# Kernel tuning notes

Measured on AMD Instinct MI355X. Metric: run time of the kernel, lower is better.

## Reference

```python
import jax, jax.numpy as jnp
import numpy as np

N, D_FEAT, D, H, L = 2048, 128, 256, 8, 2
DH = D // H
E = 65536
NUM_EDGE_TYPES = 8
MAX_DIST = 10
MAX_DEGREE = 512
D_FF = 4 * D
D_OUT = 128
EPS = 1e-5


def _layernorm(x, g, b):
    mu = jnp.mean(x, axis=-1, keepdims=True)
    var = jnp.mean(jnp.square(x - mu), axis=-1, keepdims=True)
    return (x - mu) * jax.lax.rsqrt(var + EPS) * g + b


def setup_inputs() -> dict:
    key = jax.random.key(0)
    ks = jax.random.split(key, 32)
    inp = {
        "x": jax.random.normal(ks[0], (N, D_FEAT), dtype=jnp.float32),
        "edge_index": jax.random.randint(ks[1], (2, E), 0, N),
        "edge_types": jax.random.randint(ks[2], (E,), 0, NUM_EDGE_TYPES),
        "pos_encoding": jax.random.uniform(ks[3], (N, N), dtype=jnp.float32),
    }
    def xavier(k, shape):
        fan_in, fan_out = shape[0], shape[1]
        lim = float(np.sqrt(6.0 / (fan_in + fan_out)))
        return jax.random.uniform(k, shape, jnp.float32, -lim, lim)
    inp["W_emb"] = xavier(ks[4], (D_FEAT, D)); inp["b_emb"] = jnp.zeros((D,), jnp.float32)
    # stacked per-layer params, stored as [in, out] so y = x @ W + b
    inp["Wq"] = jnp.stack([xavier(jax.random.fold_in(ks[5], l), (D, D)) for l in range(L)])
    inp["Wk"] = jnp.stack([xavier(jax.random.fold_in(ks[6], l), (D, D)) for l in range(L)])
    inp["Wv"] = jnp.stack([xavier(jax.random.fold_in(ks[7], l), (D, D)) for l in range(L)])
    inp["Wo"] = jnp.stack([xavier(jax.random.fold_in(ks[8], l), (D, D)) for l in range(L)])
    for nm in ("bq", "bk", "bv", "bo"):
        inp[nm] = jnp.zeros((L, D), jnp.float32)
    inp["spd_table"] = 0.02 * jax.random.normal(ks[9], (L, MAX_DIST + 1, H), dtype=jnp.float32)
    inp["edge_table"] = 0.02 * jax.random.normal(ks[10], (L, NUM_EDGE_TYPES, H), dtype=jnp.float32)
    inp["din_emb"] = 0.02 * jax.random.normal(ks[11], (L, MAX_DEGREE + 1, D), dtype=jnp.float32)
    inp["dout_emb"] = 0.02 * jax.random.normal(ks[12], (L, MAX_DEGREE + 1, D), dtype=jnp.float32)
    inp["ln1_g"] = jnp.ones((L, D), jnp.float32); inp["ln1_b"] = jnp.zeros((L, D), jnp.float32)
    inp["ln2_g"] = jnp.ones((L, D), jnp.float32); inp["ln2_b"] = jnp.zeros((L, D), jnp.float32)
    inp["W1"] = jnp.stack([xavier(jax.random.fold_in(ks[13], l), (D, D_FF)) for l in range(L)])
    inp["b1"] = jnp.zeros((L, D_FF), jnp.float32)
    inp["W2"] = jnp.stack([xavier(jax.random.fold_in(ks[14], l), (D_FF, D)) for l in range(L)])
    inp["b2"] = jnp.zeros((L, D), jnp.float32)
    inp["W_out"] = xavier(ks[15], (D, D_OUT)); inp["b_out"] = jnp.zeros((D_OUT,), jnp.float32)
    return inp


def _forward(x, edge_index, edge_types, pos_encoding,
             W_emb, b_emb, Wq, bq, Wk, bk, Wv, bv, Wo, bo,
             spd_table, edge_table, din_emb, dout_emb,
             ln1_g, ln1_b, ln2_g, ln2_b, W1, b1, W2, b2, W_out, b_out):
    src, dst = edge_index[0], edge_index[1]
    ones = jnp.ones((E,), jnp.int32)
    deg_out = jnp.clip(jax.ops.segment_sum(ones, src, num_segments=N), 0, MAX_DEGREE)
    deg_in = jnp.clip(jax.ops.segment_sum(ones, dst, num_segments=N), 0, MAX_DEGREE)
    # SPD bucket matrix [N, N] (int), shared across layers
    spd_bucket = jnp.clip(pos_encoding[:, :N] * MAX_DIST + 0.5, 0, MAX_DIST).astype(jnp.int32)

    h = x @ W_emb + b_emb  # node embedding; dropout=0 (eval)
    scale = 1.0 / np.sqrt(DH)
    for l in range(L):
        # centrality encoding
        h = h + din_emb[l][deg_in] + dout_emb[l][deg_out]
        xn = _layernorm(h, ln1_g[l], ln1_b[l])
        q = (xn @ Wq[l] + bq[l]).reshape(N, H, DH).transpose(1, 0, 2)  # [H,N,DH]
        k = (xn @ Wk[l] + bk[l]).reshape(N, H, DH).transpose(1, 0, 2)
        v = (xn @ Wv[l] + bv[l]).reshape(N, H, DH).transpose(1, 0, 2)
        # attention bias [H, N, N]: SPD table gather + per-edge scatter-add
        bias = spd_table[l][spd_bucket].transpose(2, 0, 1)
        e_bias = edge_table[l][edge_types]  # [E, H]
        bias = bias.at[:, src, dst].add(e_bias.T)
        scores = jnp.einsum('hnd,hmd->hnm', q, k) * scale + bias
        attn = jax.nn.softmax(scores, axis=-1)
        attn_out = jnp.einsum('hnm,hmd->hnd', attn, v).transpose(1, 0, 2).reshape(N, D)
        h = h + attn_out @ Wo[l] + bo[l]
        y = _layernorm(h, ln2_g[l], ln2_b[l])
        y = jax.nn.gelu(y @ W1[l] + b1[l], approximate=False) @ W2[l] + b2[l]
        h = h + y
    return h @ W_out + b_out


def reference(x, edge_index, edge_types, pos_encoding,
              W_emb, b_emb, Wq, bq, Wk, bk, Wv, bv, Wo, bo,
              spd_table, edge_table, din_emb, dout_emb,
              ln1_g, ln1_b, ln2_g, ln2_b, W1, b1, W2, b2, W_out, b_out):
    return _forward(x, edge_index, edge_types, pos_encoding,
                    W_emb, b_emb, Wq, bq, Wk, bk, Wv, bv, Wo, bo,
                    spd_table, edge_table, din_emb, dout_emb,
                    ln1_g, ln1_b, ln2_g, ln2_b, W1, b1, W2, b2, W_out, b_out)
```

## Files before the change

kernel.cpp:

```cpp
#include <hip/hip_runtime.h>
#include <math.h>

#define N_NODES 2048
#define D_MODEL 256
#define D_FEAT 128
#define NHEAD 8
#define DH 32
#define NLAYER 2
#define NEDGE 65536
#define D_FF 1024
#define D_OUT 128
#define MAXDEG 512
#define JSPLIT 4

typedef __attribute__((ext_vector_type(8))) short short8;
typedef __attribute__((ext_vector_type(4))) float f32x4;
typedef __attribute__((ext_vector_type(4))) unsigned short u16x4;

__device__ __forceinline__ unsigned short f2bf(float f) {
    unsigned u = __float_as_uint(f);
    unsigned r = (u + 0x7FFFu + ((u >> 16) & 1u)) >> 16;
    return (unsigned short)r;
}

template <int CTRL>
__device__ __forceinline__ float dpp_ror(float x) {
    return __int_as_float(__builtin_amdgcn_update_dpp(0, __float_as_int(x), CTRL, 0xf, 0xf, false));
}

__global__ void degree_hist_kernel(const int* __restrict__ ei,
                                   int* __restrict__ deg_out, int* __restrict__ deg_in,
                                   unsigned* __restrict__ hist) {
    int e = blockIdx.x * 256 + threadIdx.x;
    if (e < NEDGE) {
        int src = ei[e], dst = ei[NEDGE + e];
        atomicAdd(&deg_out[src], 1);
        atomicAdd(&deg_in[dst], 1);
        atomicAdd(&hist[(src >> 6) * 2048 + dst], 1);
    }
}

__global__ void edge_scan1_kernel(const unsigned* __restrict__ hist,
                                  unsigned* __restrict__ offsets, unsigned* __restrict__ blocksum) {
    __shared__ unsigned tmp[256];
    int t = threadIdx.x;
    int g = blockIdx.x * 256 + t;
    unsigned v = hist[g];
    tmp[t] = v; __syncthreads();
    for (int off = 1; off < 256; off <<= 1) {
        unsigned u = (t >= off) ? tmp[t - off] : 0;
        __syncthreads();
        tmp[t] += u;
        __syncthreads();
    }
    offsets[g] = tmp[t] - v;
    if (t == 255) blocksum[blockIdx.x] = tmp[255];
}

__global__ void edge_scan2_kernel(unsigned* __restrict__ blocksum) {
    __shared__ unsigned tmp[256];
    int t = threadIdx.x;
    unsigned v = blocksum[t];
    tmp[t] = v; __syncthreads();
    for (int off = 1; off < 256; off <<= 1) {
        unsigned u = (t >= off) ? tmp[t - off] : 0;
        __syncthreads();
        tmp[t] += u;
        __syncthreads();
    }
    blocksum[t] = tmp[t] - v;
}

__global__ void edge_scan3_kernel(const unsigned* __restrict__ blocksum,
                                  unsigned* __restrict__ offsets, unsigned* __restrict__ cursor) {
    int g = blockIdx.x * 256 + threadIdx.x;
    unsigned o = offsets[g] + blocksum[blockIdx.x];
    offsets[g] = o; cursor[g] = o;
    if (g == 0) offsets[65536] = NEDGE;
}

__global__ void edge_scatter_kernel(const int* __restrict__ ei, const int* __restrict__ etypes,
                                    unsigned* __restrict__ cursor, unsigned* __restrict__ packed) {
    int e = blockIdx.x * 256 + threadIdx.x;
    if (e < NEDGE) {
        int src = ei[e], dst = ei[NEDGE + e];
        int key = (src >> 6) * 2048 + dst;
        unsigned pos = atomicAdd(&cursor[key], 1);
        packed[pos] = (unsigned)dst | ((unsigned)(src & 63) << 11) | ((unsigned)etypes[e] << 17);
    }
}

__global__ void bucket_kernel(const float* __restrict__ pos, unsigned char* __restrict__ bucket) {
    int i = blockIdx.x * 256 + threadIdx.x;
    float4 p = *(const float4*)&pos[(size_t)i * 4];
    unsigned b0 = (unsigned)fminf(fmaxf(p.x * 10.f + 0.5f, 0.f), 10.f);
    unsigned b1 = (unsigned)fminf(fmaxf(p.y * 10.f + 0.5f, 0.f), 10.f);
    unsigned b2 = (unsigned)fminf(fmaxf(p.z * 10.f + 0.5f, 0.f), 10.f);
    unsigned b3 = (unsigned)fminf(fmaxf(p.w * 10.f + 0.5f, 0.f), 10.f);
    ((unsigned*)bucket)[i] = b0 | (b1 << 8) | (b2 << 16) | (b3 << 24);
}

__global__ void centrality_ln_kernel(float* __restrict__ h,
                                     const float* __restrict__ din_l,
                                     const float* __restrict__ dout_l,
                                     const int* __restrict__ deg_in,
                                     const int* __restrict__ deg_out,
                                     const float* __restrict__ g,
                                     const float* __restrict__ b,
                                     unsigned short* __restrict__ y) {
    int row = blockIdx.x;
    int tid = threadIdx.x;
    int di = min(deg_in[row], MAXDEG);
    int dn = min(deg_out[row], MAXDEG);
    float v = h[row * D_MODEL + tid] + din_l[di * D_MODEL + tid] + dout_l[dn * D_MODEL + tid];
    h[row * D_MODEL + tid] = v;
    __shared__ float red[256];
    red[tid] = v; __syncthreads();
    for (int s = 128; s > 0; s >>= 1) { if (tid < s) red[tid] += red[tid + s]; __syncthreads(); }
    float mu = red[0] * (1.0f / D_MODEL);
    __syncthreads();
    float d = v - mu;
    red[tid] = d * d; __syncthreads();
    for (int s = 128; s > 0; s >>= 1) { if (tid < s) red[tid] += red[tid + s]; __syncthreads(); }
    float rstd = rsqrtf(red[0] * (1.0f / D_MODEL) + 1e-5f);
    y[row * D_MODEL + tid] = f2bf(d * rstd * g[tid] + b[tid]);
}

__global__ void layernorm_kernel(const float* __restrict__ x,
                                 const float* __restrict__ g,
                                 const float* __restrict__ b,
                                 unsigned short* __restrict__ y) {
    int row = blockIdx.x;
    int tid = threadIdx.x;
    float v = x[row * D_MODEL + tid];
    __shared__ float red[256];
    red[tid] = v; __syncthreads();
    for (int s = 128; s > 0; s >>= 1) { if (tid < s) red[tid] += red[tid + s]; __syncthreads(); }
    float mu = red[0] * (1.0f / D_MODEL);
    __syncthreads();
    float d = v - mu;
    red[tid] = d * d; __syncthreads();
    for (int s = 128; s > 0; s >>= 1) { if (tid < s) red[tid] += red[tid + s]; __syncthreads(); }
    float rstd = rsqrtf(red[0] * (1.0f / D_MODEL) + 1e-5f);
    y[row * D_MODEL + tid] = f2bf(d * rstd * g[tid] + b[tid]);
}

__device__ __forceinline__ void wt_tile(const float* __restrict__ W, unsigned short* __restrict__ Wt,
                                        int K, int Nc, int n0, int k0, int tid,
                                        unsigned short (*tile)[33]) {
    int r = tid >> 3, cg = (tid & 7) * 4;
    float4 w4 = *(const float4*)&W[(size_t)(k0 + r) * Nc + n0 + cg];
    tile[r][cg + 0] = f2bf(w4.x); tile[r][cg + 1] = f2bf(w4.y);
    tile[r][cg + 2] = f2bf(w4.z); tile[r][cg + 3] = f2bf(w4.w);
    __syncthreads();
    int c = tid >> 3, rg = (tid & 7) * 4;
    u16x4 o;
    #pragma unroll
    for (int j = 0; j < 4; j++) o[j] = tile[rg + j][c];
    *(u16x4*)&Wt[(size_t)(n0 + c) * K + k0 + rg] = o;
}

__global__ void wt_all_kernel(const float* __restrict__ Wq, const float* __restrict__ Wk,
                              const float* __restrict__ Wv, const float* __restrict__ Wo,
                              const float* __restrict__ W1, const float* __restrict__ W2,
                              const float* __restrict__ W_emb, const float* __restrict__ W_out,
                              const float* __restrict__ bq, const float* __restrict__ bk,
                              const float* __restrict__ bv,
                              unsigned short* __restrict__ qkvt, unsigned short* __restrict__ wot,
                              unsigned short* __restrict__ w1t, unsigned short* __restrict__ w2t,
                              unsigned short* __restrict__ wembt, unsigned short* __restrict__ woutt,
                              float* __restrict__ bqkv) {
    __shared__ unsigned short tile[32][33];
    int b = blockIdx.x, tid = threadIdx.x;
    if (b < 512) {
        int z = b >> 6, t = b & 63;
        int l = z >> 2, which = z & 3;
        const float* W = (which == 0 ? Wq : which == 1 ? Wk : which == 2 ? Wv : Wo) + (size_t)l * 65536;
        unsigned short* dst = (which < 3) ? qkvt + (size_t)l * 196608 + which * 65536
                                          : wot + (size_t)l * 65536;
        wt_tile(W, dst, 256, 256, (t & 7) * 32, (t >> 3) * 32, tid, tile);
    } else if (b < 1024) {
        int b2 = b - 512, l = b2 >> 8, t = b2 & 255;
        wt_tile(W1 + (size_t)l * D_MODEL * D_FF, w1t + (size_t)l * D_MODEL * D_FF,
                D_MODEL, D_FF, (t & 31) * 32, (t >> 5) * 32, tid, tile);
    } else if (b < 1536) {
        int b3 = b - 1024, l = b3 >> 8, t = b3 & 255;
        wt_tile(W2 + (size_t)l * D_FF * D_MODEL, w2t + (size_t)l * D_FF * D_MODEL,
                D_FF, D_MODEL, (t & 7) * 32, (t >> 3) * 32, tid, tile);
    } else if (b < 1568) {
        int b4 = b - 1536;
        wt_tile(W_emb, wembt, D_FEAT, D_MODEL, (b4 & 7) * 32, (b4 >> 3) * 32, tid, tile);
    } else if (b < 1600) {
        int b5 = b - 1568;
        wt_tile(W_out, woutt, D_MODEL, D_OUT, (b5 & 3) * 32, (b5 >> 2) * 32, tid, tile);
    } else {
        int i = (b - 1600) * 256 + tid;
        if (i < NLAYER * 768) {
            int l = i / 768, j = i % 768;
            const float* src = j < 256 ? bq : j < 512 ? bk : bv;
            bqkv[i] = src[l * 256 + (j & 255)];
        }
    }
}

template <int ACT, bool RESID, bool OUTBF16, bool AFP32>
__global__ void gemm_mfma_kernel(const void* __restrict__ Av,
                                 const unsigned short* __restrict__ Wt,
                                 const float* __restrict__ bias,
                                 float* __restrict__ C, unsigned short* __restrict__ Cb,
                                 int Nc, int K) {
    __shared__ __align__(16) unsigned short As[32][72];
    __shared__ __align__(16) unsigned short Bs[64][72];
    const unsigned short* A16 = (const unsigned short*)Av;
    const float* A32 = (const float*)Av;
    int tid = threadIdx.x;
    int m0 = blockIdx.y * 32, n0 = blockIdx.x * 64;
    int w = tid >> 6, lane = tid & 63;
    int rg = (w & 1) * 16, cg = (w >> 1) * 32;
    int m = lane & 15, quad = lane >> 4;
    f32x4 acc[2] = {{0.f, 0.f, 0.f, 0.f}, {0.f, 0.f, 0.f, 0.f}};
    int ar = tid >> 3, ac = (tid & 7) * 8;
    uint4 ra; float4 fa0, fa1; uint4 rb0, rb1;
    if (AFP32) {
        fa0 = *(const float4*)&A32[(size_t)(m0 + ar) * K + ac];
        fa1 = *(const float4*)&A32[(size_t)(m0 + ar) * K + ac + 4];
    } else {
        ra = *(const uint4*)&A16[(size_t)(m0 + ar) * K + ac];
    }
    rb0 = *(const uint4*)&Wt[(size_t)(n0 + ar) * K + ac];
    rb1 = *(const uint4*)&Wt[(size_t)(n0 + 32 + ar) * K + ac];
    for (int k0 = 0; k0 < K; k0 += 64) {
        if (AFP32) {
            u16x4 t0 = {f2bf(fa0.x), f2bf(fa0.y), f2bf(fa0.z), f2bf(fa0.w)};
            u16x4 t1 = {f2bf(fa1.x), f2bf(fa1.y), f2bf(fa1.z), f2bf(fa1.w)};
            *(u16x4*)&As[ar][ac] = t0;
            *(u16x4*)&As[ar][ac + 4] = t1;
        } else {
            *(uint4*)&As[ar][ac] = ra;
        }
        *(uint4*)&Bs[ar][ac] = rb0;
        *(uint4*)&Bs[ar + 32][ac] = rb1;
        __syncthreads();
        int kn = k0 + 64;
        if (kn < K) {
            if (AFP32) {
                fa0 = *(const float4*)&A32[(size_t)(m0 + ar) * K + kn + ac];
                fa1 = *(const float4*)&A32[(size_t)(m0 + ar) * K + kn + ac + 4];
            } else {
                ra = *(const uint4*)&A16[(size_t)(m0 + ar) * K + kn + ac];
            }
            rb0 = *(const uint4*)&Wt[(size_t)(n0 + ar) * K + kn + ac];
            rb1 = *(const uint4*)&Wt[(size_t)(n0 + 32 + ar) * K + kn + ac];
        }
        #pragma unroll
        for (int ks = 0; ks < 2; ks++) {
            short8 a = *(const short8*)&As[rg + m][ks * 32 + quad * 8];
            #pragma unroll
            for (int t = 0; t < 2; t++) {
                short8 b = *(const short8*)&Bs[cg + t * 16 + m][ks * 32 + quad * 8];
                acc[t] = __builtin_amdgcn_mfma_f32_16x16x32_bf16(a, b, acc[t], 0, 0, 0);
            }
        }
        __syncthreads();
    }
    #pragma unroll
    for (int t = 0; t < 2; t++) {
        #pragma unroll
        for (int reg = 0; reg < 4; reg++) {
            int row = m0 + rg + quad * 4 + reg;
            int col = n0 + cg + t * 16 + m;
            float val = acc[t][reg] + bias[col];
            if (ACT == 1) val = val * 0.5f * (1.0f + erff(val * 0.7071067811865476f));
            size_t idx = (size_t)row * Nc + col;
            if (RESID) val += C[idx];
            if (OUTBF16) Cb[idx] = f2bf(val);
            else C[idx] = val;
        }
    }
}

template <int ACT, bool VBT>
__global__ void gemm64_kernel(const unsigned short* __restrict__ A,
                              const unsigned short* __restrict__ Wt,
                              const float* __restrict__ bias,
                              unsigned short* __restrict__ Cb,
                              unsigned short* __restrict__ vbt,
                              int Nc, int K) {
    __shared__ __align__(16) unsigned short As[64][72];
    __shared__ __align__(16) unsigned short Bs[64][72];
    int tid = threadIdx.x;
    int m0 = blockIdx.y * 64, n0 = blockIdx.x * 64;
    int w = tid >> 6, lane = tid & 63;
    int wr = (w & 1) * 32, wc = (w >> 1) * 32;
    int m = lane & 15, quad = lane >> 4;
    f32x4 acc[2][2] = {{{0.f,0.f,0.f,0.f},{0.f,0.f,0.f,0.f}},{{0.f,0.f,0.f,0.f},{0.f,0.f,0.f,0.f}}};
    int sr = tid >> 2, sg = (tid & 3) * 16;
    uint4 a0 = *(const uint4*)&A[(size_t)(m0 + sr) * K + sg];
    uint4 a1 = *(const uint4*)&A[(size_t)(m0 + sr) * K + sg + 8];
    uint4 b0 = *(const uint4*)&Wt[(size_t)(n0 + sr) * K + sg];
    uint4 b1 = *(const uint4*)&Wt[(size_t)(n0 + sr) * K + sg + 8];
    for (int k0 = 0; k0 < K; k0 += 64) {
        *(uint4*)&As[sr][sg] = a0;
        *(uint4*)&As[sr][sg + 8] = a1;
        *(uint4*)&Bs[sr][sg] = b0;
        *(uint4*)&Bs[sr][sg + 8] = b1;
        __syncthreads();
        int kn = k0 + 64;
        if (kn < K) {
            a0 = *(const uint4*)&A[(size_t)(m0 + sr) * K + kn + sg];
            a1 = *(const uint4*)&A[(size_t)(m0 + sr) * K + kn + sg + 8];
            b0 = *(const uint4*)&Wt[(size_t)(n0 + sr) * K + kn + sg];
            b1 = *(const uint4*)&Wt[(size_t)(n0 + sr) * K + kn + sg + 8];
        }
        #pragma unroll
        for (int kh = 0; kh < 2; kh++) {
            short8 x0 = *(const short8*)&As[wr + m][kh * 32 + quad * 8];
            short8 x1 = *(const short8*)&As[wr + 16 + m][kh * 32 + quad * 8];
            short8 y0 = *(const short8*)&Bs[wc + m][kh * 32 + quad * 8];
            short8 y1 = *(const short8*)&Bs[wc + 16 + m][kh * 32 + quad * 8];
            acc[0][0] = __builtin_amdgcn_mfma_f32_16x16x32_bf16(x0, y0, acc[0][0], 0, 0, 0);
            acc[0][1] = __builtin_amdgcn_mfma_f32_16x16x32_bf16(x0, y1, acc[0][1], 0, 0, 0);
            acc[1][0] = __builtin_amdgcn_mfma_f32_16x16x32_bf16(x1, y0, acc[1][0], 0, 0, 0);
            acc[1][1] = __builtin_amdgcn_mfma_f32_16x16x32_bf16(x1, y1, acc[1][1], 0, 0, 0);
        }
        __syncthreads();
    }
    #pragma unroll
    for (int mt = 0; mt < 2; mt++) {
        #pragma unroll
        for (int nt = 0; nt < 2; nt++) {
            #pragma unroll
            for (int reg = 0; reg < 4; reg++) {
                int row = m0 + wr + mt * 16 + quad * 4 + reg;
                int col = n0 + wc + nt * 16 + m;
                float val = acc[mt][nt][reg] + bias[col];
                if (ACT == 1) val = val * 0.5f * (1.0f + erff(val * 0.7071067811865476f));
                unsigned short bv = f2bf(val);
                Cb[(size_t)row * Nc + col] = bv;
                if (VBT && col >= 512)
                    vbt[(size_t)(col - 512) * N_NODES + row] = bv;
            }
        }
    }
}

__global__ __launch_bounds__(256)
void flash_attn_kernel(const unsigned short* __restrict__ qkvb,
                       const unsigned short* __restrict__ vbt,
                       const unsigned char* __restrict__ bucket,
                       const float* __restrict__ spd_l,
                       const float* __restrict__ et_l,
                       const unsigned* __restrict__ offsets,
                       const unsigned* __restrict__ packed,
                       float* __restrict__ part_O,
                       float* __restrict__ m_part, float* __restrict__ l_part) {
    __shared__ __align__(16) unsigned short ks[64][40];
    __shared__ __align__(16) unsigned short vs[32][72];
    __shared__ __align__(16) float ov[64][68];
    __shared__ float et[8];

    int tid = threadIdx.x;
    int rb = blockIdx.x;
    int i0 = rb * 64;
    int hh = blockIdx.y;
    int js = blockIdx.z;
    int lane = tid & 63;
    if (tid < 8) et[tid] = et_l[tid * NHEAD + hh];
    float spd_reg = spd_l[(lane < 11 ? lane : 10) * NHEAD + hh];

    int w = tid >> 6;
    int m = lane & 15, quad = lane >> 4;
    int r0 = w * 16;
    short8 aq = *(const short8*)&qkvb[(size_t)(i0 + r0 + m) * 768 + hh * DH + quad * 8];
    float m_st[4], l_st[4];
    #pragma unroll
    for (int r = 0; r < 4; r++) { m_st[r] = -3.0e38f; l_st[r] = 0.f; }
    f32x4 oacc[2] = {{0.f, 0.f, 0.f, 0.f}, {0.f, 0.f, 0.f, 0.f}};
    const float scale = 0.17677669529663687f;

    int krow = tid >> 2, kcol = (tid & 3) * 8;
    int vrow = tid >> 3, vcol = (tid & 7) * 8;
    int brow = tid >> 2, bcol = (tid & 3) * 16;

    for (int jt = 0; jt < N_NODES / JSPLIT / 64; jt++) {
        int j0 = js * (N_NODES / JSPLIT) + jt * 64;
        __syncthreads();
        *(uint4*)&ks[krow][kcol] =
            *(const uint4*)&qkvb[(size_t)(j0 + krow) * 768 + 256 + hh * DH + kcol];
        *(uint4*)&vs[vrow][vcol] =
            *(const uint4*)&vbt[(size_t)(hh * DH + vrow) * N_NODES + j0 + vcol];
        {
            uint4 b16 = *(const uint4*)&bucket[(size_t)(i0 + brow) * N_NODES + j0 + bcol];
            const unsigned char* bb = (const unsigned char*)&b16;
            float fb[16];
            #pragma unroll
            for (int i = 0; i < 16; i++)
                fb[i] = __int_as_float(
                    __builtin_amdgcn_ds_bpermute(((int)bb[i]) << 2, __float_as_int(spd_reg)));
            #pragma unroll
            for (int g = 0; g < 4; g++) {
                f32x4 st = {fb[g * 4], fb[g * 4 + 1], fb[g * 4 + 2], fb[g * 4 + 3]};
                *(f32x4*)&ov[brow][bcol + g * 4] = st;
            }
        }
        __syncthreads();
        {
            unsigned key0 = (unsigned)rb * 2048 + j0;
            unsigned start = offsets[key0], end = offsets[key0 + 64];
            for (unsigned i = start + tid; i < end; i += 256) {
                unsigned p = packed[i];
                atomicAdd(&ov[(p >> 11) & 63][(p & 2047) - j0], et[(p >> 17) & 7]);
            }
        }
        __syncthreads();
        float sv[4][4];
        #pragma unroll
        for (int t = 0; t < 4; t++) {
            short8 bk8 = *(const short8*)&ks[t * 16 + m][quad * 8];
            f32x4 z = {0.f, 0.f, 0.f, 0.f};
            f32x4 sacc = __builtin_amdgcn_mfma_f32_16x16x32_bf16(aq, bk8, z, 0, 0, 0);
            #pragma unroll
            for (int r = 0; r < 4; r++)
                sv[t][r] = sacc[r] * scale + ov[r0 + quad * 4 + r][t * 16 + m];
        }
        float alpha[4];
        #pragma unroll
        for (int r = 0; r < 4; r++) {
            float mx = fmaxf(fmaxf(sv[0][r], sv[1][r]), fmaxf(sv[2][r], sv[3][r]));
            mx = fmaxf(mx, dpp_ror<0x121>(mx));
            mx = fmaxf(mx, dpp_ror<0x122>(mx));
            mx = fmaxf(mx, dpp_ror<0x124>(mx));
            mx = fmaxf(mx, dpp_ror<0x128>(mx));
            float mn = fmaxf(m_st[r], mx);
            alpha[r] = __expf(m_st[r] - mn);
            m_st[r] = mn;
            float ps = 0.f;
            #pragma unroll
            for (int t = 0; t < 4; t++) { float pv = __expf(sv[t][r] - mn); sv[t][r] = pv; ps += pv; }
            ps += dpp_ror<0x121>(ps);
            ps += dpp_ror<0x122>(ps);
            ps += dpp_ror<0x124>(ps);
            ps += dpp_ror<0x128>(ps);
            l_st[r] = l_st[r] * alpha[r] + ps;
        }
        #pragma unroll
        for (int t = 0; t < 4; t++)
            #pragma unroll
            for (int r = 0; r < 4; r++)
                ov[r0 + quad * 4 + r][t * 16 + m] = sv[t][r];
        #pragma unroll
        for (int r = 0; r < 4; r++) { oacc[0][r] *= alpha[r]; oacc[1][r] *= alpha[r]; }
        __builtin_amdgcn_s_waitcnt(0xC07F);
        #pragma unroll
        for (int kh = 0; kh < 2; kh++) {
            f32x4 p0 = *(const f32x4*)&ov[r0 + m][kh * 32 + quad * 8];
            f32x4 p1 = *(const f32x4*)&ov[r0 + m][kh * 32 + quad * 8 + 4];
            short8 pa;
            pa[0] = (short)f2bf(p0[0]); pa[1] = (short)f2bf(p0[1]);
            pa[2] = (short)f2bf(p0[2]); pa[3] = (short)f2bf(p0[3]);
            pa[4] = (short)f2bf(p1[0]); pa[5] = (short)f2bf(p1[1]);
            pa[6] = (short)f2bf(p1[2]); pa[7] = (short)f2bf(p1[3]);
            #pragma unroll
            for (int t = 0; t < 2; t++) {
                short8 vb = *(const short8*)&vs[t * 16 + m][kh * 32 + quad * 8];
                oacc[t] = __builtin_amdgcn_mfma_f32_16x16x32_bf16(pa, vb, oacc[t], 0, 0, 0);
            }
        }
    }
    #pragma unroll
    for (int t = 0; t < 2; t++)
        #pragma unroll
        for (int r = 0; r < 4; r++)
            part_O[((size_t)js * N_NODES + i0 + r0 + quad * 4 + r) * D_MODEL + hh * DH + t * 16 + m] =
                oacc[t][r];
    if (m == 0) {
        #pragma unroll
        for (int r = 0; r < 4; r++) {
            int row = i0 + r0 + quad * 4 + r;
            m_part[((size_t)js * NHEAD + hh) * N_NODES + row] = m_st[r];
            l_part[((size_t)js * NHEAD + hh) * N_NODES + row] = l_st[r];
        }
    }
}

__global__ void flash_merge_kernel(const float* __restrict__ part_O,
                                   const float* __restrict__ m_part,
                                   const float* __restrict__ l_part,
                                   unsigned short* __restrict__ aoutb) {
    int e = blockIdx.x * 256 + threadIdx.x;
    int row = e >> 8, col = e & 255, h = col >> 5;
    float mv[JSPLIT];
    float mg = -3.0e38f;
    #pragma unroll
    for (int js = 0; js < JSPLIT; js++) {
        mv[js] = m_part[((size_t)js * NHEAD + h) * N_NODES + row];
        mg = fmaxf(mg, mv[js]);
    }
    float o = 0.f, l = 0.f;
    #pragma unroll
    for (int js = 0; js < JSPLIT; js++) {
        float sc = __expf(mv[js] - mg);
        o += sc * part_O[(size_t)js * N_NODES * D_MODEL + e];
        l += sc * l_part[((size_t)js * NHEAD + h) * N_NODES + row];
    }
    aoutb[e] = f2bf(o / l);
}

extern "C" void kernel_launch(void* const* d_in, const int* in_sizes, int n_in,
                              void* d_out, int out_size, void* d_ws, size_t ws_size,
                              hipStream_t stream) {
    const float* x          = (const float*)d_in[0];
    const int*   edge_index = (const int*)d_in[1];
    const int*   edge_types = (const int*)d_in[2];
    const float* pos        = (const float*)d_in[3];
    const float* W_emb      = (const float*)d_in[4];
    const float* b_emb      = (const float*)d_in[5];
    const float* Wq         = (const float*)d_in[6];
    const float* Wk         = (const float*)d_in[7];
    const float* Wv         = (const float*)d_in[8];
    const float* Wo         = (const float*)d_in[9];
    const float* bq         = (const float*)d_in[10];
    const float* bk         = (const float*)d_in[11];
    const float* bv         = (const float*)d_in[12];
    const float* bo         = (const float*)d_in[13];
    const float* spd_table  = (const float*)d_in[14];
    const float* edge_table = (const float*)d_in[15];
    const float* din_emb    = (const float*)d_in[16];
    const float* dout_emb   = (const float*)d_in[17];
    const float* ln1_g      = (const float*)d_in[18];
    const float* ln1_b      = (const float*)d_in[19];
    const float* ln2_g      = (const float*)d_in[20];
    const float* ln2_b      = (const float*)d_in[21];
    const float* W1         = (const float*)d_in[22];
    const float* b1         = (const float*)d_in[23];
    const float* W2         = (const float*)d_in[24];
    const float* b2         = (const float*)d_in[25];
    const float* W_out      = (const float*)d_in[26];
    const float* b_out      = (const float*)d_in[27];
    float* out = (float*)d_out;

    char* base = (char*)d_ws;
    int* deg_out = (int*)base;                    base += (size_t)N_NODES * 4;
    int* deg_in  = (int*)base;                    base += (size_t)N_NODES * 4;
    float* h     = (float*)base;                  base += (size_t)N_NODES * D_MODEL * 4;
    unsigned short* xb   = (unsigned short*)base; base += (size_t)N_NODES * D_MODEL * 2;
    unsigned short* qkvb = (unsigned short*)base; base += (size_t)N_NODES * 768 * 2;
    unsigned short* vbt  = (unsigned short*)base; base += (size_t)D_MODEL * N_NODES * 2;
    unsigned short* aoutb = (unsigned short*)base; base += (size_t)N_NODES * D_MODEL * 2;
    unsigned short* ffnb = (unsigned short*)base; base += (size_t)N_NODES * D_FF * 2;
    unsigned char* bucket = (unsigned char*)base; base += (size_t)N_NODES * N_NODES;
    unsigned short* qkvt = (unsigned short*)base; base += (size_t)NLAYER * 768 * D_MODEL * 2;
    unsigned short* wot  = (unsigned short*)base; base += (size_t)NLAYER * D_MODEL * D_MODEL * 2;
    unsigned short* w1t  = (unsigned short*)base; base += (size_t)NLAYER * D_MODEL * D_FF * 2;
    unsigned short* w2t  = (unsigned short*)base; base += (size_t)NLAYER * D_FF * D_MODEL * 2;
    unsigned short* wembt = (unsigned short*)base; base += (size_t)D_FEAT * D_MODEL * 2;
    unsigned short* woutt = (unsigned short*)base; base += (size_t)D_MODEL * D_OUT * 2;
    float* bqkv = (float*)base;                   base += (size_t)NLAYER * 768 * 4;
    unsigned* hist    = (unsigned*)base;          base += (size_t)65536 * 4;
    unsigned* offsets = (unsigned*)base;          base += (size_t)65537 * 4;
    unsigned* cursor  = (unsigned*)base;          base += (size_t)65536 * 4;
    unsigned* blocksum = (unsigned*)base;         base += (size_t)256 * 4;
    unsigned* packed  = (unsigned*)base;          base += (size_t)NEDGE * 4;
    float* part_O = (float*)base;                 base += (size_t)JSPLIT * N_NODES * D_MODEL * 4;
    float* m_part = (float*)base;                 base += (size_t)JSPLIT * NHEAD * N_NODES * 4;
    float* l_part = (float*)base;                 base += (size_t)JSPLIT * NHEAD * N_NODES * 4;

    hipMemsetAsync(deg_out, 0, (size_t)N_NODES * 4 * 2, stream);
    hipMemsetAsync(hist, 0, (size_t)65536 * 4, stream);

    degree_hist_kernel<<<NEDGE / 256, 256, 0, stream>>>(edge_index, deg_out, deg_in, hist);
    edge_scan1_kernel<<<256, 256, 0, stream>>>(hist, offsets, blocksum);
    edge_scan2_kernel<<<1, 256, 0, stream>>>(blocksum);
    edge_scan3_kernel<<<256, 256, 0, stream>>>(blocksum, offsets, cursor);
    edge_scatter_kernel<<<NEDGE / 256, 256, 0, stream>>>(edge_index, edge_types, cursor, packed);
    wt_all_kernel<<<1606, 256, 0, stream>>>(Wq, Wk, Wv, Wo, W1, W2, W_emb, W_out,
                                            bq, bk, bv, qkvt, wot, w1t, w2t, wembt, woutt, bqkv);
    bucket_kernel<<<(size_t)N_NODES * N_NODES / 4 / 256, 256, 0, stream>>>(pos, bucket);

    gemm_mfma_kernel<0, false, false, true><<<dim3(D_MODEL / 64, N_NODES / 32), 256, 0, stream>>>(
        x, wembt, b_emb, h, nullptr, D_MODEL, D_FEAT);

    for (int l = 0; l < NLAYER; l++) {
        centrality_ln_kernel<<<N_NODES, 256, 0, stream>>>(
            h, din_emb + (size_t)l * (MAXDEG + 1) * D_MODEL,
            dout_emb + (size_t)l * (MAXDEG + 1) * D_MODEL, deg_in, deg_out,
            ln1_g + l * D_MODEL, ln1_b + l * D_MODEL, xb);

        gemm64_kernel<0, true><<<dim3(768 / 64, N_NODES / 64), 256, 0, stream>>>(
            xb, qkvt + (size_t)l * 768 * D_MODEL, bqkv + l * 768, qkvb, vbt, 768, D_MODEL);

        flash_attn_kernel<<<dim3(N_NODES / 64, NHEAD, JSPLIT), 256, 0, stream>>>(
            qkvb, vbt, bucket, spd_table + (size_t)l * 11 * NHEAD,
            edge_table + (size_t)l * 8 * NHEAD, offsets, packed, part_O, m_part, l_part);

        flash_merge_kernel<<<N_NODES * D_MODEL / 256, 256, 0, stream>>>(part_O, m_part, l_part, aoutb);

        gemm_mfma_kernel<0, true, false, false><<<dim3(D_MODEL / 64, N_NODES / 32), 256, 0, stream>>>(
            aoutb, wot + (size_t)l * D_MODEL * D_MODEL, bo + l * D_MODEL, h, nullptr, D_MODEL, D_MODEL);

        layernorm_kernel<<<N_NODES, 256, 0, stream>>>(h, ln2_g + l * D_MODEL, ln2_b + l * D_MODEL, xb);

        gemm64_kernel<1, false><<<dim3(D_FF / 64, N_NODES / 64), 256, 0, stream>>>(
            xb, w1t + (size_t)l * D_MODEL * D_FF, b1 + l * D_FF, ffnb, nullptr, D_FF, D_MODEL);

        gemm_mfma_kernel<0, true, false, false><<<dim3(D_MODEL / 64, N_NODES / 32), 256, 0, stream>>>(
            ffnb, w2t + (size_t)l * D_FF * D_MODEL, b2 + l * D_MODEL, h, nullptr, D_MODEL, D_FF);
    }

    gemm_mfma_kernel<0, false, false, true><<<dim3(D_OUT / 64, N_NODES / 32), 256, 0, stream>>>(
        h, woutt, b_out, out, nullptr, D_OUT, D_MODEL);
}
```

Baseline: 314.4 us.

## Fuse prep kernels, merge flash split-K in-kernel, split-K atomic residual GEMMs

Merges the bucket, weight-transpose, bias-pack and memset work into one prep kernel, and collapses the three-pass edge scan into a single 1024-thread block. The flash-attention merge now runs inside the attention kernel: the last split to finish for each (row-block, head) does the merge, tracked by an atomic counter. The Wo and W2 residual GEMMs use split-K over a z grid dimension with float atomicAdd into h. The goal is fewer launches and more parallelism for small GEMMs, at the cost of atomic contention and non-deterministic summation order.

```diff
diff --git a/kernel.cpp b/kernel.cpp
--- a/kernel.cpp
+++ b/kernel.cpp
@@ -28,6 +28,89 @@
     return __int_as_float(__builtin_amdgcn_update_dpp(0, __float_as_int(x), CTRL, 0xf, 0xf, false));
 }
 
+__device__ __forceinline__ void wt_tile(const float* __restrict__ W, unsigned short* __restrict__ Wt,
+                                        int K, int Nc, int n0, int k0, int tid,
+                                        unsigned short (*tile)[33]) {
+    int r = tid >> 3, cg = (tid & 7) * 4;
+    float4 w4 = *(const float4*)&W[(size_t)(k0 + r) * Nc + n0 + cg];
+    tile[r][cg + 0] = f2bf(w4.x); tile[r][cg + 1] = f2bf(w4.y);
+    tile[r][cg + 2] = f2bf(w4.z); tile[r][cg + 3] = f2bf(w4.w);
+    __syncthreads();
+    int c = tid >> 3, rg = (tid & 7) * 4;
+    u16x4 o;
+    #pragma unroll
+    for (int j = 0; j < 4; j++) o[j] = tile[rg + j][c];
+    *(u16x4*)&Wt[(size_t)(n0 + c) * K + k0 + rg] = o;
+}
+
+__global__ void mega_prep_kernel(const float* __restrict__ pos, unsigned char* __restrict__ bucket,
+                                 unsigned* __restrict__ hist, int* __restrict__ deg_out,
+                                 int* __restrict__ deg_in, unsigned* __restrict__ cnt,
+                                 const float* __restrict__ Wq, const float* __restrict__ Wk,
+                                 const float* __restrict__ Wv, const float* __restrict__ Wo,
+                                 const float* __restrict__ W1, const float* __restrict__ W2,
+                                 const float* __restrict__ W_emb, const float* __restrict__ W_out,
+                                 const float* __restrict__ bq, const float* __restrict__ bk,
+                                 const float* __restrict__ bv,
+                                 unsigned short* __restrict__ qkvt, unsigned short* __restrict__ wot,
+                                 unsigned short* __restrict__ w1t, unsigned short* __restrict__ w2t,
+                                 unsigned short* __restrict__ wembt, unsigned short* __restrict__ woutt,
+                                 float* __restrict__ bqkv) {
+    __shared__ unsigned short tile[32][33];
+    int b = blockIdx.x, tid = threadIdx.x;
+    if (b < 4096) {
+        int i = b * 256 + tid;
+        float4 p = *(const float4*)&pos[(size_t)i * 4];
+        unsigned b0 = (unsigned)fminf(fmaxf(p.x * 10.f + 0.5f, 0.f), 10.f);
+        unsigned b1 = (unsigned)fminf(fmaxf(p.y * 10.f + 0.5f, 0.f), 10.f);
+        unsigned b2 = (unsigned)fminf(fmaxf(p.z * 10.f + 0.5f, 0.f), 10.f);
+        unsigned b3 = (unsigned)fminf(fmaxf(p.w * 10.f + 0.5f, 0.f), 10.f);
+        ((unsigned*)bucket)[i] = b0 | (b1 << 8) | (b2 << 16) | (b3 << 24);
+        if (b < 64) {
+            #pragma unroll
+            for (int k = 0; k < 4; k++) hist[b * 1024 + k * 256 + tid] = 0;
+        } else if (b == 64) {
+            #pragma unroll
+            for (int k = 0; k < 8; k++) deg_out[k * 256 + tid] = 0;
+            #pragma unroll
+            for (int k = 0; k < 8; k++) deg_in[k * 256 + tid] = 0;
+        } else if (b == 65) {
+            cnt[tid] = 0; cnt[256 + tid] = 0;
+        }
+        return;
+    }
+    int bb = b - 4096;
+    if (bb < 512) {
+        int z = bb >> 6, t = bb & 63;
+        int l = z >> 2, which = z & 3;
+        const float* W = (which == 0 ? Wq : which == 1 ? Wk : which == 2 ? Wv : Wo) + (size_t)l * 65536;
+        unsigned short* dst = (which < 3) ? qkvt + (size_t)l * 196608 + which * 65536
+                                          : wot + (size_t)l * 65536;
+        wt_tile(W, dst, 256, 256, (t & 7) * 32, (t >> 3) * 32, tid, tile);
+    } else if (bb < 1024) {
+        int b2 = bb - 512, l = b2 >> 8, t = b2 & 255;
+        wt_tile(W1 + (size_t)l * D_MODEL * D_FF, w1t + (size_t)l * D_MODEL * D_FF,
+                D_MODEL, D_FF, (t & 31) * 32, (t >> 5) * 32, tid, tile);
+    } else if (bb < 1536) {
+        int b3 = bb - 1024, l = b3 >> 8, t = b3 & 255;
+        wt_tile(W2 + (size_t)l * D_FF * D_MODEL, w2t + (size_t)l * D_FF * D_MODEL,
+                D_FF, D_MODEL, (t & 7) * 32, (t >> 3) * 32, tid, tile);
+    } else if (bb < 1568) {
+        int b4 = bb - 1536;
+        wt_tile(W_emb, wembt, D_FEAT, D_MODEL, (b4 & 7) * 32, (b4 >> 3) * 32, tid, tile);
+    } else if (bb < 1600) {
+        int b5 = bb - 1568;
+        wt_tile(W_out, woutt, D_MODEL, D_OUT, (b5 & 3) * 32, (b5 >> 2) * 32, tid, tile);
+    } else {
+        int i = (bb - 1600) * 256 + tid;
+        if (i < NLAYER * 768) {
+            int l = i / 768, j = i % 768;
+            const float* src = j < 256 ? bq : j < 512 ? bk : bv;
+            bqkv[i] = src[l * 256 + (j & 255)];
+        }
+    }
+}
+
 __global__ void degree_hist_kernel(const int* __restrict__ ei,
                                    int* __restrict__ deg_out, int* __restrict__ deg_in,
                                    unsigned* __restrict__ hist) {
@@ -40,43 +123,27 @@
     }
 }
 
-__global__ void edge_scan1_kernel(const unsigned* __restrict__ hist,
-                                  unsigned* __restrict__ offsets, unsigned* __restrict__ blocksum) {
-    __shared__ unsigned tmp[256];
+__global__ void edge_scan_all_kernel(const unsigned* __restrict__ hist,
+                                     unsigned* __restrict__ offsets, unsigned* __restrict__ cursor) {
+    __shared__ unsigned tmp[1024];
     int t = threadIdx.x;
-    int g = blockIdx.x * 256 + t;
-    unsigned v = hist[g];
-    tmp[t] = v; __syncthreads();
-    for (int off = 1; off < 256; off <<= 1) {
+    unsigned s = 0;
+    for (int i = 0; i < 64; i++) s += hist[t * 64 + i];
+    tmp[t] = s;
+    __syncthreads();
+    for (int off = 1; off < 1024; off <<= 1) {
         unsigned u = (t >= off) ? tmp[t - off] : 0;
         __syncthreads();
         tmp[t] += u;
         __syncthreads();
     }
-    offsets[g] = tmp[t] - v;
-    if (t == 255) blocksum[blockIdx.x] = tmp[255];
-}
-
-__global__ void edge_scan2_kernel(unsigned* __restrict__ blocksum) {
-    __shared__ unsigned tmp[256];
-    int t = threadIdx.x;
-    unsigned v = blocksum[t];
-    tmp[t] = v; __syncthreads();
-    for (int off = 1; off < 256; off <<= 1) {
-        unsigned u = (t >= off) ? tmp[t - off] : 0;
-        __syncthreads();
-        tmp[t] += u;
-        __syncthreads();
-    }
-    blocksum[t] = tmp[t] - v;
-}
-
-__global__ void edge_scan3_kernel(const unsigned* __restrict__ blocksum,
-                                  unsigned* __restrict__ offsets, unsigned* __restrict__ cursor) {
-    int g = blockIdx.x * 256 + threadIdx.x;
-    unsigned o = offsets[g] + blocksum[blockIdx.x];
-    offsets[g] = o; cursor[g] = o;
-    if (g == 0) offsets[65536] = NEDGE;
+    unsigned run = tmp[t] - s;
+    for (int i = 0; i < 64; i++) {
+        int g = t * 64 + i;
+        offsets[g] = run; cursor[g] = run;
+        run += hist[g];
+    }
+    if (t == 1023) offsets[65536] = NEDGE;
 }
 
 __global__ void edge_scatter_kernel(const int* __restrict__ ei, const int* __restrict__ etypes,
@@ -88,16 +155,6 @@
         unsigned pos = atomicAdd(&cursor[key], 1);
         packed[pos] = (unsigned)dst | ((unsigned)(src & 63) << 11) | ((unsigned)etypes[e] << 17);
     }
-}
-
-__global__ void bucket_kernel(const float* __restrict__ pos, unsigned char* __restrict__ bucket) {
-    int i = blockIdx.x * 256 + threadIdx.x;
-    float4 p = *(const float4*)&pos[(size_t)i * 4];
-    unsigned b0 = (unsigned)fminf(fmaxf(p.x * 10.f + 0.5f, 0.f), 10.f);
-    unsigned b1 = (unsigned)fminf(fmaxf(p.y * 10.f + 0.5f, 0.f), 10.f);
-    unsigned b2 = (unsigned)fminf(fmaxf(p.z * 10.f + 0.5f, 0.f), 10.f);
-    unsigned b3 = (unsigned)fminf(fmaxf(p.w * 10.f + 0.5f, 0.f), 10.f);
-    ((unsigned*)bucket)[i] = b0 | (b1 << 8) | (b2 << 16) | (b3 << 24);
 }
 
 __global__ void centrality_ln_kernel(float* __restrict__ h,
@@ -110,8 +167,8 @@
                                      unsigned short* __restrict__ y) {
     int row = blockIdx.x;
     int tid = threadIdx.x;
-    int di = min(deg_in[row], MAXDEG);
-    int dn = min(deg_out[row], MAXDEG);
+    int di = min(max(deg_in[row], 0), MAXDEG);
+    int dn = min(max(deg_out[row], 0), MAXDEG);
     float v = h[row * D_MODEL + tid] + din_l[di * D_MODEL + tid] + dout_l[dn * D_MODEL + tid];
     h[row * D_MODEL + tid] = v;
     __shared__ float red[256];
@@ -145,65 +202,7 @@
     y[row * D_MODEL + tid] = f2bf(d * rstd * g[tid] + b[tid]);
 }
 
-__device__ __forceinline__ void wt_tile(const float* __restrict__ W, unsigned short* __restrict__ Wt,
-                                        int K, int Nc, int n0, int k0, int tid,
-                                        unsigned short (*tile)[33]) {
-    int r = tid >> 3, cg = (tid & 7) * 4;
-    float4 w4 = *(const float4*)&W[(size_t)(k0 + r) * Nc + n0 + cg];
-    tile[r][cg + 0] = f2bf(w4.x); tile[r][cg + 1] = f2bf(w4.y);
-    tile[r][cg + 2] = f2bf(w4.z); tile[r][cg + 3] = f2bf(w4.w);
-    __syncthreads();
-    int c = tid >> 3, rg = (tid & 7) * 4;
-    u16x4 o;
-    #pragma unroll
-    for (int j = 0; j < 4; j++) o[j] = tile[rg + j][c];
-    *(u16x4*)&Wt[(size_t)(n0 + c) * K + k0 + rg] = o;
-}
-
-__global__ void wt_all_kernel(const float* __restrict__ Wq, const float* __restrict__ Wk,
-                              const float* __restrict__ Wv, const float* __restrict__ Wo,
-                              const float* __restrict__ W1, const float* __restrict__ W2,
-                              const float* __restrict__ W_emb, const float* __restrict__ W_out,
-                              const float* __restrict__ bq, const float* __restrict__ bk,
-                              const float* __restrict__ bv,
-                              unsigned short* __restrict__ qkvt, unsigned short* __restrict__ wot,
-                              unsigned short* __restrict__ w1t, unsigned short* __restrict__ w2t,
-                              unsigned short* __restrict__ wembt, unsigned short* __restrict__ woutt,
-                              float* __restrict__ bqkv) {
-    __shared__ unsigned short tile[32][33];
-    int b = blockIdx.x, tid = threadIdx.x;
-    if (b < 512) {
-        int z = b >> 6, t = b & 63;
-        int l = z >> 2, which = z & 3;
-        const float* W = (which == 0 ? Wq : which == 1 ? Wk : which == 2 ? Wv : Wo) + (size_t)l * 65536;
-        unsigned short* dst = (which < 3) ? qkvt + (size_t)l * 196608 + which * 65536
-                                          : wot + (size_t)l * 65536;
-        wt_tile(W, dst, 256, 256, (t & 7) * 32, (t >> 3) * 32, tid, tile);
-    } else if (b < 1024) {
-        int b2 = b - 512, l = b2 >> 8, t = b2 & 255;
-        wt_tile(W1 + (size_t)l * D_MODEL * D_FF, w1t + (size_t)l * D_MODEL * D_FF,
-                D_MODEL, D_FF, (t & 31) * 32, (t >> 5) * 32, tid, tile);
-    } else if (b < 1536) {
-        int b3 = b - 1024, l = b3 >> 8, t = b3 & 255;
-        wt_tile(W2 + (size_t)l * D_FF * D_MODEL, w2t + (size_t)l * D_FF * D_MODEL,
-                D_FF, D_MODEL, (t & 7) * 32, (t >> 3) * 32, tid, tile);
-    } else if (b < 1568) {
-        int b4 = b - 1536;
-        wt_tile(W_emb, wembt, D_FEAT, D_MODEL, (b4 & 7) * 32, (b4 >> 3) * 32, tid, tile);
-    } else if (b < 1600) {
-        int b5 = b - 1568;
-        wt_tile(W_out, woutt, D_MODEL, D_OUT, (b5 & 3) * 32, (b5 >> 2) * 32, tid, tile);
-    } else {
-        int i = (b - 1600) * 256 + tid;
-        if (i < NLAYER * 768) {
-            int l = i / 768, j = i % 768;
-            const float* src = j < 256 ? bq : j < 512 ? bk : bv;
-            bqkv[i] = src[l * 256 + (j & 255)];
-        }
-    }
-}
-
-template <int ACT, bool RESID, bool OUTBF16, bool AFP32>
+template <int ACT, bool RESID, bool OUTBF16, bool AFP32, bool ATOMIC>
 __global__ void gemm_mfma_kernel(const void* __restrict__ Av,
                                  const unsigned short* __restrict__ Wt,
                                  const float* __restrict__ bias,
@@ -215,6 +214,9 @@
     const float* A32 = (const float*)Av;
     int tid = threadIdx.x;
     int m0 = blockIdx.y * 32, n0 = blockIdx.x * 64;
+    int kz = blockIdx.z;
+    int Ksub = K / gridDim.z;
+    int kbase = kz * Ksub;
     int w = tid >> 6, lane = tid & 63;
     int rg = (w & 1) * 16, cg = (w >> 1) * 32;
     int m = lane & 15, quad = lane >> 4;
@@ -222,14 +224,14 @@
     int ar = tid >> 3, ac = (tid & 7) * 8;
     uint4 ra; float4 fa0, fa1; uint4 rb0, rb1;
     if (AFP32) {
-        fa0 = *(const float4*)&A32[(size_t)(m0 + ar) * K + ac];
-        fa1 = *(const float4*)&A32[(size_t)(m0 + ar) * K + ac + 4];
+        fa0 = *(const float4*)&A32[(size_t)(m0 + ar) * K + kbase + ac];
+        fa1 = *(const float4*)&A32[(size_t)(m0 + ar) * K + kbase + ac + 4];
     } else {
-        ra = *(const uint4*)&A16[(size_t)(m0 + ar) * K + ac];
-    }
-    rb0 = *(const uint4*)&Wt[(size_t)(n0 + ar) * K + ac];
-    rb1 = *(const uint4*)&Wt[(size_t)(n0 + 32 + ar) * K + ac];
-    for (int k0 = 0; k0 < K; k0 += 64) {
+        ra = *(const uint4*)&A16[(size_t)(m0 + ar) * K + kbase + ac];
+    }
+    rb0 = *(const uint4*)&Wt[(size_t)(n0 + ar) * K + kbase + ac];
+    rb1 = *(const uint4*)&Wt[(size_t)(n0 + 32 + ar) * K + kbase + ac];
+    for (int k0 = kbase; k0 < kbase + Ksub; k0 += 64) {
         if (AFP32) {
             u16x4 t0 = {f2bf(fa0.x), f2bf(fa0.y), f2bf(fa0.z), f2bf(fa0.w)};
             u16x4 t1 = {f2bf(fa1.x), f2bf(fa1.y), f2bf(fa1.z), f2bf(fa1.w)};
@@ -242,7 +244,7 @@
         *(uint4*)&Bs[ar + 32][ac] = rb1;
         __syncthreads();
         int kn = k0 + 64;
-        if (kn < K) {
+        if (kn < kbase + Ksub) {
             if (AFP32) {
                 fa0 = *(const float4*)&A32[(size_t)(m0 + ar) * K + kn + ac];
                 fa1 = *(const float4*)&A32[(size_t)(m0 + ar) * K + kn + ac + 4];
@@ -269,12 +271,17 @@
         for (int reg = 0; reg < 4; reg++) {
             int row = m0 + rg + quad * 4 + reg;
             int col = n0 + cg + t * 16 + m;
-            float val = acc[t][reg] + bias[col];
-            if (ACT == 1) val = val * 0.5f * (1.0f + erff(val * 0.7071067811865476f));
             size_t idx = (size_t)row * Nc + col;
-            if (RESID) val += C[idx];
-            if (OUTBF16) Cb[idx] = f2bf(val);
-            else C[idx] = val;
+            if (ATOMIC) {
+                float val = acc[t][reg] + (kz == 0 ? bias[col] : 0.f);
+                atomicAdd(&C[idx], val);
+            } else {
+                float val = acc[t][reg] + bias[col];
+                if (ACT == 1) val = val * 0.5f * (1.0f + erff(val * 0.7071067811865476f));
+                if (RESID) val += C[idx];
+                if (OUTBF16) Cb[idx] = f2bf(val);
+                else C[idx] = val;
+            }
         }
     }
 }
@@ -353,11 +360,14 @@
                        const unsigned* __restrict__ offsets,
                        const unsigned* __restrict__ packed,
                        float* __restrict__ part_O,
-                       float* __restrict__ m_part, float* __restrict__ l_part) {
+                       float* __restrict__ m_part, float* __restrict__ l_part,
+                       unsigned* __restrict__ cnt,
+                       unsigned short* __restrict__ aoutb) {
     __shared__ __align__(16) unsigned short ks[64][40];
     __shared__ __align__(16) unsigned short vs[32][72];
     __shared__ __align__(16) float ov[64][68];
     __shared__ float et[8];
+    __shared__ unsigned lastflag;
 
     int tid = threadIdx.x;
     int rb = blockIdx.x;
@@ -481,30 +491,45 @@
             l_part[((size_t)js * NHEAD + hh) * N_NODES + row] = l_st[r];
         }
     }
-}
-
-__global__ void flash_merge_kernel(const float* __restrict__ part_O,
-                                   const float* __restrict__ m_part,
-                                   const float* __restrict__ l_part,
-                                   unsigned short* __restrict__ aoutb) {
-    int e = blockIdx.x * 256 + threadIdx.x;
-    int row = e >> 8, col = e & 255, h = col >> 5;
-    float mv[JSPLIT];
-    float mg = -3.0e38f;
-    #pragma unroll
-    for (int js = 0; js < JSPLIT; js++) {
-        mv[js] = m_part[((size_t)js * NHEAD + h) * N_NODES + row];
-        mg = fmaxf(mg, mv[js]);
-    }
-    float o = 0.f, l = 0.f;
-    #pragma unroll
-    for (int js = 0; js < JSPLIT; js++) {
-        float sc = __expf(mv[js] - mg);
-        o += sc * part_O[(size_t)js * N_NODES * D_MODEL + e];
-        l += sc * l_part[((size_t)js * NHEAD + h) * N_NODES + row];
-    }
-    aoutb[e] = f2bf(o / l);
-}
+    __threadfence();
+    if (tid == 0)
+        lastflag = (atomicAdd(&cnt[rb * NHEAD + hh], 1) == JSPLIT - 1) ? 1u : 0u;
+    __syncthreads();
+    if (lastflag) {
+        __threadfence();
+        int r = tid >> 2;
+        int dg = (tid & 3) * 8;
+        float mv[JSPLIT];
+        float mg = -3.0e38f;
+        #pragma unroll
+        for (int s = 0; s < JSPLIT; s++) {
+            mv[s] = m_part[((size_t)s * NHEAD + hh) * N_NODES + i0 + r];
+            mg = fmaxf(mg, mv[s]);
+        }
+        float l = 0.f;
+        float o[8] = {0.f, 0.f, 0.f, 0.f, 0.f, 0.f, 0.f, 0.f};
+        #pragma unroll
+        for (int s = 0; s < JSPLIT; s++) {
+            float sc = __expf(mv[s] - mg);
+            l += sc * l_part[((size_t)s * NHEAD + hh) * N_NODES + i0 + r];
+            const float* pp = &part_O[((size_t)s * N_NODES + i0 + r) * D_MODEL + hh * DH + dg];
+            float4 p0 = *(const float4*)pp;
+            float4 p1 = *(const float4*)(pp + 4);
+            o[0] += sc * p0.x; o[1] += sc * p0.y; o[2] += sc * p0.z; o[3] += sc * p0.w;
+            o[4] += sc * p1.x; o[5] += sc * p1.y; o[6] += sc * p1.z; o[7] += sc * p1.w;
+        }
+        float inv = 1.0f / l;
+        u16x4 q0, q1;
+        #pragma unroll
+        for (int k = 0; k < 4; k++) { q0[k] = f2bf(o[k] * inv); q1[k] = f2bf(o[k + 4] * inv); }
+        unsigned short* dst = &aoutb[(size_t)(i0 + r) * D_MODEL + hh * DH + dg];
+        *(u16x4*)dst = q0;
+        *(u16x4*)(dst + 4) = q1;
+    }
+}
+
+#define WS_ALLOC(type, name, count) \
+    type* name = (type*)base; base += (((size_t)(count) * sizeof(type)) + 255) & ~(size_t)255;
 
 extern "C" void kernel_launch(void* const* d_in, const int* in_sizes, int n_in,
                               void* d_out, int out_size, void* d_ws, size_t ws_size,
@@ -540,44 +565,39 @@
     float* out = (float*)d_out;
 
     char* base = (char*)d_ws;
-    int* deg_out = (int*)base;                    base += (size_t)N_NODES * 4;
-    int* deg_in  = (int*)base;                    base += (size_t)N_NODES * 4;
-    float* h     = (float*)base;                  base += (size_t)N_NODES * D_MODEL * 4;
-    unsigned short* xb   = (unsigned short*)base; base += (size_t)N_NODES * D_MODEL * 2;
-    unsigned short* qkvb = (unsigned short*)base; base += (size_t)N_NODES * 768 * 2;
-    unsigned short* vbt  = (unsigned short*)base; base += (size_t)D_MODEL * N_NODES * 2;
-    unsigned short* aoutb = (unsigned short*)base; base += (size_t)N_NODES * D_MODEL * 2;
-    unsigned short* ffnb = (unsigned short*)base; base += (size_t)N_NODES * D_FF * 2;
-    unsigned char* bucket = (unsigned char*)base; base += (size_t)N_NODES * N_NODES;
-    unsigned short* qkvt = (unsigned short*)base; base += (size_t)NLAYER * 768 * D_MODEL * 2;
-    unsigned short* wot  = (unsigned short*)base; base += (size_t)NLAYER * D_MODEL * D_MODEL * 2;
-    unsigned short* w1t  = (unsigned short*)base; base += (size_t)NLAYER * D_MODEL * D_FF * 2;
-    unsigned short* w2t  = (unsigned short*)base; base += (size_t)NLAYER * D_FF * D_MODEL * 2;
-    unsigned short* wembt = (unsigned short*)base; base += (size_t)D_FEAT * D_MODEL * 2;
-    unsigned short* woutt = (unsigned short*)base; base += (size_t)D_MODEL * D_OUT * 2;
-    float* bqkv = (float*)base;                   base += (size_t)NLAYER * 768 * 4;
-    unsigned* hist    = (unsigned*)base;          base += (size_t)65536 * 4;
-    unsigned* offsets = (unsigned*)base;          base += (size_t)65537 * 4;
-    unsigned* cursor  = (unsigned*)base;          base += (size_t)65536 * 4;
-    unsigned* blocksum = (unsigned*)base;         base += (size_t)256 * 4;
-    unsigned* packed  = (unsigned*)base;          base += (size_t)NEDGE * 4;
-    float* part_O = (float*)base;                 base += (size_t)JSPLIT * N_NODES * D_MODEL * 4;
-    float* m_part = (float*)base;                 base += (size_t)JSPLIT * NHEAD * N_NODES * 4;
-    float* l_part = (float*)base;                 base += (size_t)JSPLIT * NHEAD * N_NODES * 4;
-
-    hipMemsetAsync(deg_out, 0, (size_t)N_NODES * 4 * 2, stream);
-    hipMemsetAsync(hist, 0, (size_t)65536 * 4, stream);
-
+    WS_ALLOC(int, deg_out, N_NODES)
+    WS_ALLOC(int, deg_in, N_NODES)
+    WS_ALLOC(float, h, N_NODES * D_MODEL)
+    WS_ALLOC(unsigned short, xb, N_NODES * D_MODEL)
+    WS_ALLOC(unsigned short, qkvb, N_NODES * 768)
+    WS_ALLOC(unsigned short, vbt, D_MODEL * N_NODES)
+    WS_ALLOC(unsigned short, aoutb, N_NODES * D_MODEL)
+    WS_ALLOC(unsigned short, ffnb, N_NODES * D_FF)
+    WS_ALLOC(unsigned char, bucket, (size_t)N_NODES * N_NODES)
+    WS_ALLOC(unsigned short, qkvt, NLAYER * 768 * D_MODEL)
+    WS_ALLOC(unsigned short, wot, NLAYER * D_MODEL * D_MODEL)
+    WS_ALLOC(unsigned short, w1t, NLAYER * D_MODEL * D_FF)
+    WS_ALLOC(unsigned short, w2t, NLAYER * D_FF * D_MODEL)
+    WS_ALLOC(unsigned short, wembt, D_FEAT * D_MODEL)
+    WS_ALLOC(unsigned short, woutt, D_MODEL * D_OUT)
+    WS_ALLOC(float, bqkv, NLAYER * 768)
+    WS_ALLOC(unsigned, hist, 65536)
+    WS_ALLOC(unsigned, offsets, 65537)
+    WS_ALLOC(unsigned, cursor, 65536)
+    WS_ALLOC(unsigned, cnt, NLAYER * 256)
+    WS_ALLOC(unsigned, packed, NEDGE)
+    WS_ALLOC(float, part_O, (size_t)JSPLIT * N_NODES * D_MODEL)
+    WS_ALLOC(float, m_part, (size_t)JSPLIT * NHEAD * N_NODES)
+    WS_ALLOC(float, l_part, (size_t)JSPLIT * NHEAD * N_NODES)
+
+    mega_prep_kernel<<<5702, 256, 0, stream>>>(pos, bucket, hist, deg_out, deg_in, cnt,
+                                               Wq, Wk, Wv, Wo, W1, W2, W_emb, W_out,
+                                               bq, bk, bv, qkvt, wot, w1t, w2t, wembt, woutt, bqkv);
     degree_hist_kernel<<<NEDGE / 256, 256, 0, stream>>>(edge_index, deg_out, deg_in, hist);
-    edge_scan1_kernel<<<256, 256, 0, stream>>>(hist, offsets, blocksum);
-    edge_scan2_kernel<<<1, 256, 0, stream>>>(blocksum);
-    edge_scan3_kernel<<<256, 256, 0, stream>>>(blocksum, offsets, cursor);
+    edge_scan_all_kernel<<<1, 1024, 0, stream>>>(hist, offsets, cursor);
     edge_scatter_kernel<<<NEDGE / 256, 256, 0, stream>>>(edge_index, edge_types, cursor, packed);
-    wt_all_kernel<<<1606, 256, 0, stream>>>(Wq, Wk, Wv, Wo, W1, W2, W_emb, W_out,
-                                            bq, bk, bv, qkvt, wot, w1t, w2t, wembt, woutt, bqkv);
-    bucket_kernel<<<(size_t)N_NODES * N_NODES / 4 / 256, 256, 0, stream>>>(pos, bucket);
-
-    gemm_mfma_kernel<0, false, false, true><<<dim3(D_MODEL / 64, N_NODES / 32), 256, 0, stream>>>(
+
+    gemm_mfma_kernel<0, false, false, true, false><<<dim3(D_MODEL / 64, N_NODES / 32), 256, 0, stream>>>(
         x, wembt, b_emb, h, nullptr, D_MODEL, D_FEAT);
 
     for (int l = 0; l < NLAYER; l++) {
@@ -591,11 +611,10 @@
 
         flash_attn_kernel<<<dim3(N_NODES / 64, NHEAD, JSPLIT), 256, 0, stream>>>(
             qkvb, vbt, bucket, spd_table + (size_t)l * 11 * NHEAD,
-            edge_table + (size_t)l * 8 * NHEAD, offsets, packed, part_O, m_part, l_part);
-
-        flash_merge_kernel<<<N_NODES * D_MODEL / 256, 256, 0, stream>>>(part_O, m_part, l_part, aoutb);
-
-        gemm_mfma_kernel<0, true, false, false><<<dim3(D_MODEL / 64, N_NODES / 32), 256, 0, stream>>>(
+            edge_table + (size_t)l * 8 * NHEAD, offsets, packed, part_O, m_part, l_part,
+            cnt + l * 256, aoutb);
+
+        gemm_mfma_kernel<0, false, false, false, true><<<dim3(D_MODEL / 64, N_NODES / 32, 2), 256, 0, stream>>>(
             aoutb, wot + (size_t)l * D_MODEL * D_MODEL, bo + l * D_MODEL, h, nullptr, D_MODEL, D_MODEL);
 
         layernorm_kernel<<<N_NODES, 256, 0, stream>>>(h, ln2_g + l * D_MODEL, ln2_b + l * D_MODEL, xb);
@@ -603,10 +622,10 @@
         gemm64_kernel<1, false><<<dim3(D_FF / 64, N_NODES / 64), 256, 0, stream>>>(
             xb, w1t + (size_t)l * D_MODEL * D_FF, b1 + l * D_FF, ffnb, nullptr, D_FF, D_MODEL);
 
-        gemm_mfma_kernel<0, true, false, false><<<dim3(D_MODEL / 64, N_NODES / 32), 256, 0, stream>>>(
+        gemm_mfma_kernel<0, false, false, false, true><<<dim3(D_MODEL / 64, N_NODES / 32, 4), 256, 0, stream>>>(
             ffnb, w2t + (size_t)l * D_FF * D_MODEL, b2 + l * D_MODEL, h, nullptr, D_MODEL, D_FF);
     }
 
-    gemm_mfma_kernel<0, false, false, true><<<dim3(D_OUT / 64, N_NODES / 32), 256, 0, stream>>>(
+    gemm_mfma_kernel<0, false, false, true, false><<<dim3(D_OUT / 64, N_NODES / 32), 256, 0, stream>>>(
         h, woutt, b_out, out, nullptr, D_OUT, D_MODEL);
 }
```

After: 573.8 us. 82.5% more time.
